# Performance work log

Measured on AMD Instinct MI355X. Metric: run time of the kernel, lower is better.

## Reference

```python
import jax, jax.numpy as jnp
import numpy as np

D, FIN1, CL1_F, CL1_K, CL2_F, CL2_K, FC1_F, FC2_F = 4096, 1, 32, 25, 64, 25, 512, 10
B = 64
NNZ1, NNZ2 = D * 8, (D // 2) * 8
LMAX = 2.0  # lmax_L of a normalized graph Laplacian
FC1FIN = CL2_F * (D // 4)


def setup_inputs() -> dict:
    key = jax.random.key(0)
    ks = jax.random.split(key, 16)
    def lin(kw, fout, fin):
        scale = np.sqrt(2.0 / (fin + fout)).astype(np.float32)
        return jax.random.uniform(kw, (fout, fin), jnp.float32, -scale, scale)
    V2 = D // 2
    return {
        "x": jax.random.normal(ks[0], (B, D, FIN1), jnp.float32),
        "L1_rows": jax.random.randint(ks[1], (NNZ1,), 0, D),
        "L1_cols": jax.random.randint(ks[2], (NNZ1,), 0, D),
        "L1_vals": jax.random.normal(ks[3], (NNZ1,), jnp.float32) * 0.1,
        "L2_rows": jax.random.randint(ks[4], (NNZ2,), 0, V2),
        "L2_cols": jax.random.randint(ks[5], (NNZ2,), 0, V2),
        "L2_vals": jax.random.normal(ks[6], (NNZ2,), jnp.float32) * 0.1,
        "cl1_W": lin(ks[7], CL1_F, CL1_K * FIN1),
        "cl1_b": jnp.zeros((CL1_F,), jnp.float32),
        "cl2_W": lin(ks[8], CL2_F, CL2_K * CL1_F),
        "cl2_b": jnp.zeros((CL2_F,), jnp.float32),
        "fc1_W": lin(ks[9], FC1_F, FC1FIN),
        "fc1_b": jnp.zeros((FC1_F,), jnp.float32),
        "fc2_W": lin(ks[10], FC2_F, FC1_F),
        "fc2_b": jnp.zeros((FC2_F,), jnp.float32),
    }


def _cheby_conv(x, rows, cols, vals, W, b, K):
    # x: [B, V, Fin]; sparse rescaled Laplacian Ls = (2/lmax)*L - I applied as SpMM.
    Bn, V, Fin = x.shape
    x0 = jnp.transpose(x, (1, 2, 0)).reshape(V, Fin * Bn)  # [V, Fin*B]
    coef = jnp.asarray(2.0 / LMAX, x.dtype)

    def Ls(z):  # (2/lmax) * L @ z - z, via segment-sum SpMM
        return coef * jax.ops.segment_sum(vals[:, None] * z[cols], rows, num_segments=V) - z

    xs = [x0]
    if K > 1:
        x1 = Ls(x0)
        xs.append(x1)
    for _ in range(2, K):
        x2 = 2.0 * Ls(x1) - x0
        xs.append(x2)
        x0, x1 = x1, x2
    xk = jnp.stack(xs, 0).reshape(K, V, Fin, Bn)        # [K, V, Fin, B]
    xk = jnp.transpose(xk, (3, 1, 2, 0)).reshape(Bn * V, Fin * K)
    y = xk @ W.T + b
    return y.reshape(Bn, V, -1)


def _max_pool(x, p):
    # max-pool over node dim with stride p (matches MaxPool1d over permuted layout)
    Bn, V, F = x.shape
    return x.reshape(Bn, V // p, p, F).max(axis=2)


def reference(x, L1_rows, L1_cols, L1_vals, L2_rows, L2_cols, L2_vals,
              cl1_W, cl1_b, cl2_W, cl2_b, fc1_W, fc1_b, fc2_W, fc2_b):
    h = _cheby_conv(x, L1_rows, L1_cols, L1_vals, cl1_W, cl1_b, CL1_K)
    h = jax.nn.relu(h)
    h = _max_pool(h, 2)
    h = _cheby_conv(h, L2_rows, L2_cols, L2_vals, cl2_W, cl2_b, CL2_K)
    h = jax.nn.relu(h)
    h = _max_pool(h, 2)
    h = h.reshape(-1, FC1FIN)
    h = jax.nn.relu(h @ fc1_W.T + fc1_b)
    # dropout d=0.0 (eval/deterministic) -> identity
    return h @ fc2_W.T + fc2_b
```

## Files before the change

### kernel.cpp

```cpp
#include <hip/hip_runtime.h>
#include <hip/hip_bf16.h>

#define V1 4096
#define V2 2048
#define NNZ1 32768
#define NNZ2 16384
#define WCAP 48

typedef unsigned short u16;
typedef unsigned int u32;
typedef __attribute__((ext_vector_type(8))) short bf16x8;
typedef __attribute__((ext_vector_type(4))) float f32x4;

static __device__ __forceinline__ float bf2f(u16 u) {
  union { u32 i; float f; } c; c.i = ((u32)u) << 16; return c.f;
}
static __device__ __forceinline__ u16 f2bf(float f) {
  union { u32 i; float f; } c; c.f = f;
  u32 r = c.i + 0x7FFFu + ((c.i >> 16) & 1u);
  return (u16)(r >> 16);
}

__global__ void k_hist(const int* __restrict__ L1r, const int* __restrict__ L2r,
                       const float* __restrict__ W2, u16* __restrict__ Wh,
                       u16* __restrict__ Wl,
                       int* __restrict__ cnt1, int* __restrict__ cnt2) {
  int lt = blockIdx.x, t = threadIdx.x;
  if (lt < 128) {
    atomicAdd(&cnt1[L1r[lt * 256 + t]], 1);
  } else if (lt < 192) {
    atomicAdd(&cnt2[L2r[(lt - 128) * 256 + t]], 1);
  } else {
    int idx = (lt - 192) * 256 + t;
    int f = idx / 800;
    int kap = idx - f * 800;
    int k = kap >> 5, fin = kap & 31;
    float w = W2[f * 800 + fin * 25 + k];
    u16 hi = f2bf(w);
    Wh[idx] = hi;
    Wl[idx] = f2bf(w - bf2f(hi));
  }
}

__global__ void k_scan(int* __restrict__ cnt1, int* __restrict__ rs1,
                       int* __restrict__ cnt2, int* __restrict__ rs2,
                       int* __restrict__ slotOf1, int* __restrict__ rowOf1,
                       int* __restrict__ slotOf2, int* __restrict__ rowOf2) {
  __shared__ int sums[256];
  __shared__ int degS[V1];
  __shared__ int hist[64];
  __shared__ int hb[64];
  int t = threadIdx.x;
  int* cnt; int* rs; int* slotOf; int* rowOf; int V, NT, nnz;
  if (blockIdx.x == 0) { cnt = cnt1; rs = rs1; slotOf = slotOf1; rowOf = rowOf1; V = V1; NT = 1024; nnz = NNZ1; }
  else                 { cnt = cnt2; rs = rs2; slotOf = slotOf2; rowOf = rowOf2; V = V2; NT = 512;  nnz = NNZ2; }
  int chunk = V / 256, base = t * chunk, s = 0;
  for (int i = 0; i < chunk; ++i) { int c = cnt[base + i]; degS[base + i] = c; s += c; }
  sums[t] = s;
  if (t < 64) hist[t] = 0;
  __syncthreads();
  if (t == 0) {
    int run = 0;
    for (int i = 0; i < 256; ++i) { int c = sums[i]; sums[i] = run; run += c; }
  }
  __syncthreads();
  int pfx = sums[t];
  for (int i = 0; i < chunk; ++i) {
    int c = degS[base + i];
    rs[base + i] = pfx;
    cnt[base + i] = pfx;
    pfx += c;
  }
  if (t == 0) rs[V] = nnz;
  for (int i = 0; i < chunk; ++i) {
    int d = degS[base + i]; if (d > 63) d = 63;
    atomicAdd(&hist[d], 1);
  }
  __syncthreads();
  if (t == 0) {
    int run = 0;
    for (int d = 63; d >= 0; --d) { hb[d] = run; run += hist[d]; }
  }
  __syncthreads();
  for (int i = 0; i < chunk; ++i) {
    int v = base + i;
    int d = degS[v]; if (d > 63) d = 63;
    int r = atomicAdd(&hb[d], 1);
    int slot = (r & 3) * NT + (r >> 2);
    slotOf[v] = slot;
    rowOf[slot] = v;
  }
}

__global__ void k_scatter(const int* __restrict__ L1r, const int* __restrict__ L1c,
                          const float* __restrict__ L1v,
                          const int* __restrict__ L2r, const int* __restrict__ L2c,
                          const float* __restrict__ L2v,
                          int* __restrict__ cur1, const int* __restrict__ rs1,
                          const int* __restrict__ slotOf1, float2* __restrict__ ell1,
                          int* __restrict__ cur2, const int* __restrict__ rs2,
                          const int* __restrict__ slotOf2, float2* __restrict__ ell2) {
  int lt = blockIdx.x, t = threadIdx.x;
  if (lt < 128) {
    int e = lt * 256 + t;
    int row = L1r[e];
    int pos = atomicAdd(&cur1[row], 1);
    int w = pos - rs1[row];
    if (w < WCAP)
      ell1[(size_t)w * V1 + slotOf1[row]] = make_float2(L1v[e], __int_as_float(L1c[e] * 4));
  } else {
    int e = (lt - 128) * 256 + t;
    int row = L2r[e];
    int pos = atomicAdd(&cur2[row], 1);
    int w = pos - rs2[row];
    if (w < WCAP)
      ell2[(size_t)w * V2 + slotOf2[row]] = make_float2(L2v[e], __int_as_float(L2c[e] * 16));
  }
}

__global__ void __launch_bounds__(1024) k_l1rec(
    const float* __restrict__ x, const int* __restrict__ rs1,
    const int* __restrict__ rowOf1, const float2* __restrict__ ell1,
    u16* __restrict__ T1) {
  __shared__ float fa[V1];
  const int b = blockIdx.x, t = threadIdx.x;
#pragma unroll
  for (int j = 0; j < 4; ++j) {
    int v = t + j * 1024;
    float xv = x[(size_t)b * V1 + v];
    fa[v] = xv;
    T1[((size_t)b) * V1 + v] = f2bf(xv);
  }
  int vj[4];
#pragma unroll
  for (int j = 0; j < 4; ++j) vj[j] = rowOf1[t + j * 1024];
  int bound = rs1[vj[0] + 1] - rs1[vj[0]];
  if (bound > WCAP) bound = WCAP;
  float t2r[4];
  __syncthreads();
  for (int k = 1; k < 25; ++k) {
    float acc[4] = {0.f, 0.f, 0.f, 0.f};
    for (int w = 0; w < bound; ++w) {
      const float2* ep = ell1 + (size_t)w * V1 + t;
#pragma unroll
      for (int j = 0; j < 4; ++j) {
        float2 ev = ep[j * 1024];
        int ub = __float_as_int(ev.y);
        float av = *(const float*)((const char*)fa + ub);
        acc[j] = fmaf(ev.x, av, acc[j]);
      }
    }
    __syncthreads();
#pragma unroll
    for (int j = 0; j < 4; ++j) {
      float old = fa[vj[j]];
      float z = acc[j] - old;
      if (k > 1) z = 2.f * z - t2r[j];
      t2r[j] = old;
      fa[vj[j]] = z;
    }
    __syncthreads();
#pragma unroll
    for (int j = 0; j < 4; ++j) {
      int v = t + j * 1024;
      T1[((size_t)k * 64 + b) * V1 + v] = f2bf(fa[v]);
    }
  }
}

__global__ void k_conv1(const u16* __restrict__ T1, const float* __restrict__ W1,
                        const float* __restrict__ b1, float* __restrict__ z0) {
  __shared__ float w1s[800];
  __shared__ float b1s[32];
  const int b = blockIdx.x & 63, uc = blockIdx.x >> 6, t = threadIdx.x;
  for (int idx = t; idx < 800; idx += 256) w1s[idx] = W1[idx];
  if (t < 32) b1s[t] = b1[t];
  __syncthreads();
  const int u = uc * 256 + t;
  float a1[25], a2[25];
#pragma unroll
  for (int k = 0; k < 25; ++k) {
    u32 w = *(const u32*)&T1[((size_t)k * 64 + b) * V1 + 2 * u];
    a1[k] = bf2f((u16)w);
    a2[k] = bf2f((u16)(w >> 16));
  }
  float mout[32];
#pragma unroll
  for (int f = 0; f < 32; ++f) {
    float s1 = b1s[f], s2 = b1s[f];
#pragma unroll
    for (int k = 0; k < 25; ++k) {
      float w = w1s[f * 25 + k];
      s1 = fmaf(a1[k], w, s1);
      s2 = fmaf(a2[k], w, s2);
    }
    mout[f] = fmaxf(fmaxf(s1, 0.f), fmaxf(s2, 0.f));
  }
  float4* dst = (float4*)&z0[((size_t)b * V2 + u) * 32];
#pragma unroll
  for (int q = 0; q < 8; ++q)
    dst[q] = make_float4(mout[4 * q], mout[4 * q + 1], mout[4 * q + 2], mout[4 * q + 3]);
}

__global__ void __launch_bounds__(512, 4) k_l2rec(
    const float* __restrict__ z0, const int* __restrict__ rs2,
    const int* __restrict__ rowOf2, const float2* __restrict__ ell2,
    u16* __restrict__ T2, int b0, int bs) {
  __shared__ float TkS[V2 * 4];
  const int bl = blockIdx.x % bs, fg = blockIdx.x / bs;
  const int b = b0 + bl, f0 = fg * 4;
  const int t = threadIdx.x;
  const size_t M = (size_t)bs * V2;
  const size_t mb = (size_t)bl * V2;
#pragma unroll
  for (int j = 0; j < 4; ++j) {
    int v = t + j * 512;
    float4 xv = *(const float4*)&z0[((size_t)b * V2 + v) * 32 + f0];
    *(float4*)&TkS[v * 4] = xv;
    u32 lo = (u32)f2bf(xv.x) | ((u32)f2bf(xv.y) << 16);
    u32 hi = (u32)f2bf(xv.z) | ((u32)f2bf(xv.w) << 16);
    *(uint2*)&T2[((size_t)fg * M + mb + v) * 4] = make_uint2(lo, hi);
  }
  int vj[4];
#pragma unroll
  for (int j = 0; j < 4; ++j) vj[j] = rowOf2[t + j * 512];
  int bound = rs2[vj[0] + 1] - rs2[vj[0]];
  if (bound > WCAP) bound = WCAP;
  float4 t2r[4];
  __syncthreads();
  for (int k = 1; k < 25; ++k) {
    float4 acc[4];
#pragma unroll
    for (int j = 0; j < 4; ++j) acc[j] = make_float4(0.f, 0.f, 0.f, 0.f);
    for (int w = 0; w < bound; ++w) {
      const float2* ep = ell2 + (size_t)w * V2 + t;
#pragma unroll
      for (int j = 0; j < 4; ++j) {
        float2 ev = ep[j * 512];
        int ub = __float_as_int(ev.y);
        float4 tv = *(const float4*)((const char*)TkS + ub);
        acc[j].x = fmaf(ev.x, tv.x, acc[j].x);
        acc[j].y = fmaf(ev.x, tv.y, acc[j].y);
        acc[j].z = fmaf(ev.x, tv.z, acc[j].z);
        acc[j].w = fmaf(ev.x, tv.w, acc[j].w);
      }
    }
    __syncthreads();
#pragma unroll
    for (int j = 0; j < 4; ++j) {
      float4 old = *(const float4*)&TkS[vj[j] * 4];
      float4 z;
      z.x = acc[j].x - old.x; z.y = acc[j].y - old.y;
      z.z = acc[j].z - old.z; z.w = acc[j].w - old.w;
      if (k > 1) {
        z.x = 2.f * z.x - t2r[j].x; z.y = 2.f * z.y - t2r[j].y;
        z.z = 2.f * z.z - t2r[j].z; z.w = 2.f * z.w - t2r[j].w;
      }
      t2r[j] = old;
      *(float4*)&TkS[vj[j] * 4] = z;
    }
    __syncthreads();
#pragma unroll
    for (int j = 0; j < 4; ++j) {
      int v = t + j * 512;
      float4 zz = *(const float4*)&TkS[v * 4];
      u32 lo = (u32)f2bf(zz.x) | ((u32)f2bf(zz.y) << 16);
      u32 hi = (u32)f2bf(zz.z) | ((u32)f2bf(zz.w) << 16);
      *(uint2*)&T2[(((size_t)k * 8 + fg) * M + mb + v) * 4] = make_uint2(lo, hi);
    }
  }
}

__global__ void __launch_bounds__(256) k_conv2mm(
    const u16* __restrict__ T2, const u16* __restrict__ Wh, const u16* __restrict__ Wl,
    const float* __restrict__ b2, float* __restrict__ h2T, int b0, int bs) {
  const int t = threadIdx.x;
  const int wid = t >> 6, lane = t & 63;
  const int ln = lane & 15, kg = lane >> 4;
  const size_t M = (size_t)bs * V2;
  const int mBlk = blockIdx.x * 128;
  const int bl = mBlk >> 11;
  const int v0 = mBlk & (V2 - 1);
  const int m0 = mBlk + wid * 32;
  const int vw = v0 + wid * 32;

  f32x4 acc[2][4];
#pragma unroll
  for (int nt = 0; nt < 4; ++nt) {
    float bv = b2[nt * 16 + ln];
    acc[0][nt] = (f32x4){bv, bv, bv, bv};
    acc[1][nt] = acc[0][nt];
  }

  for (int kc = 0; kc < 25; ++kc) {
    const int coff = kc * 32 + kg * 8;
    bf16x8 bh[4], blo[4];
#pragma unroll
    for (int nt = 0; nt < 4; ++nt) {
      bh[nt]  = *(const bf16x8*)(Wh + (size_t)(nt * 16 + ln) * 800 + coff);
      blo[nt] = *(const bf16x8*)(Wl + (size_t)(nt * 16 + ln) * 800 + coff);
    }
#pragma unroll
    for (int sp = 0; sp < 2; ++sp) {
      const u16* ap = T2 + ((size_t)(kc * 8 + kg * 2) * M + (size_t)(m0 + sp * 16 + ln)) * 4;
      uint2 alo = *(const uint2*)ap;
      uint2 ahi = *(const uint2*)(ap + M * 4);
      union { uint4 u; bf16x8 v; } ac;
      ac.u = make_uint4(alo.x, alo.y, ahi.x, ahi.y);
#pragma unroll
      for (int nt = 0; nt < 4; ++nt) {
        acc[sp][nt] = __builtin_amdgcn_mfma_f32_16x16x32_bf16(ac.v, bh[nt], acc[sp][nt], 0, 0, 0);
        acc[sp][nt] = __builtin_amdgcn_mfma_f32_16x16x32_bf16(ac.v, blo[nt], acc[sp][nt], 0, 0, 0);
      }
    }
  }
  const int b = b0 + bl;
#pragma unroll
  for (int sp = 0; sp < 2; ++sp) {
    int u = ((vw + sp * 16) >> 1) + kg * 2;
#pragma unroll
    for (int nt = 0; nt < 4; ++nt) {
      int f = nt * 16 + ln;
      float p0 = fmaxf(fmaxf(acc[sp][nt].x, acc[sp][nt].y), 0.f);
      float p1 = fmaxf(fmaxf(acc[sp][nt].z, acc[sp][nt].w), 0.f);
      h2T[((size_t)u * 64 + f) * 64 + b] = p0;
      h2T[((size_t)(u + 1) * 64 + f) * 64 + b] = p1;
    }
  }
}

__global__ void k_fc1(const float* __restrict__ h2T, const float* __restrict__ fW1,
                      float* __restrict__ fc1o) {
  __shared__ float wS[16 * 256];
  const int jt = blockIdx.x & 31, ks = blockIdx.x >> 5;
  const int j0 = jt * 16, k0 = ks * 2048;
  const int t = threadIdx.x;
  const int b = t & 63, jl = t >> 6;
  float acc[4] = {0.f, 0.f, 0.f, 0.f};
  for (int kc = 0; kc < 8; ++kc) {
    int kbase = k0 + kc * 256;
    __syncthreads();
    for (int fi = t; fi < 1024; fi += 256) {
      int rowj = fi >> 6, colq = fi & 63;
      *(float4*)&wS[rowj * 256 + colq * 4] =
          *(const float4*)&fW1[(size_t)(j0 + rowj) * 65536 + kbase + colq * 4];
    }
    __syncthreads();
    for (int kl = 0; kl < 256; ++kl) {
      float hv = h2T[(size_t)(kbase + kl) * 64 + b];
#pragma unroll
      for (int q = 0; q < 4; ++q) acc[q] = fmaf(hv, wS[(jl * 4 + q) * 256 + kl], acc[q]);
    }
  }
#pragma unroll
  for (int q = 0; q < 4; ++q) atomicAdd(&fc1o[(j0 + jl * 4 + q) * 64 + b], acc[q]);
}

__global__ void k_fc2(const float* __restrict__ fc1o, const float* __restrict__ fb1,
                      const float* __restrict__ fW2, const float* __restrict__ fb2,
                      float* __restrict__ out) {
  const int c = blockIdx.x, b = threadIdx.x;
  float s = fb2[c];
  for (int j = 0; j < 512; ++j) {
    float a = fmaxf(fc1o[j * 64 + b] + fb1[j], 0.f);
    s = fmaf(a, fW2[c * 512 + j], s);
  }
  out[b * 10 + c] = s;
}

extern "C" void kernel_launch(void* const* d_in, const int* in_sizes, int n_in,
                              void* d_out, int out_size, void* d_ws, size_t ws_size,
                              hipStream_t stream) {
  const float* x    = (const float*)d_in[0];
  const int* L1r    = (const int*)d_in[1];
  const int* L1c    = (const int*)d_in[2];
  const float* L1v  = (const float*)d_in[3];
  const int* L2r    = (const int*)d_in[4];
  const int* L2c    = (const int*)d_in[5];
  const float* L2v  = (const float*)d_in[6];
  const float* W1   = (const float*)d_in[7];
  const float* b1   = (const float*)d_in[8];
  const float* W2   = (const float*)d_in[9];
  const float* b2   = (const float*)d_in[10];
  const float* fW1  = (const float*)d_in[11];
  const float* fb1  = (const float*)d_in[12];
  const float* fW2  = (const float*)d_in[13];
  const float* fb2  = (const float*)d_in[14];
  float* out = (float*)d_out;

  float* Wf = (float*)d_ws;
  size_t off = 0;
  auto alloc = [&](size_t n) { float* q = Wf + off; off += n; return q; };
  int* cnt1    = (int*)alloc(4096);
  int* rs1     = (int*)alloc(4104);
  int* cnt2    = (int*)alloc(2048);
  int* rs2     = (int*)alloc(2056);
  int* slotOf1 = (int*)alloc(4096);
  int* rowOf1  = (int*)alloc(4096);
  int* slotOf2 = (int*)alloc(2048);
  int* rowOf2  = (int*)alloc(2048);
  u16* Wh      = (u16*)alloc(25600);
  u16* Wl      = (u16*)alloc(25600);
  float* fc1o  = alloc(32768);
  float2* ell1 = (float2*)alloc((size_t)WCAP * V1 * 2);
  float2* ell2 = (float2*)alloc((size_t)WCAP * V2 * 2);
  float* z0    = alloc(4194304);
  float* h2T   = alloc(4194304);
  size_t fixedB = off * 4;

  int ns = 8;
  for (int c = 1; c <= 8; c <<= 1) {
    size_t t2b = (size_t)V2 * (64 / c) * 800 * 2;
    size_t big = t2b > 16777216ull ? t2b : 16777216ull;
    if (fixedB + big + 65536 <= ws_size) { ns = c; break; }
  }
  const int bs = 64 / ns;
  u16* T1 = (u16*)(Wf + off);
  u16* T2 = (u16*)(Wf + off);

  hipMemsetAsync(cnt1, 0, 4096 * sizeof(int), stream);
  hipMemsetAsync(cnt2, 0, 2048 * sizeof(int), stream);
  hipMemsetAsync(fc1o, 0, 32768 * sizeof(float), stream);
  hipMemsetAsync(ell1, 0, (size_t)WCAP * V1 * 8, stream);
  hipMemsetAsync(ell2, 0, (size_t)WCAP * V2 * 8, stream);

  k_hist<<<392, 256, 0, stream>>>(L1r, L2r, W2, Wh, Wl, cnt1, cnt2);
  k_scan<<<2, 256, 0, stream>>>(cnt1, rs1, cnt2, rs2, slotOf1, rowOf1, slotOf2, rowOf2);
  k_scatter<<<192, 256, 0, stream>>>(L1r, L1c, L1v, L2r, L2c, L2v,
                                     cnt1, rs1, slotOf1, ell1,
                                     cnt2, rs2, slotOf2, ell2);

  k_l1rec<<<64, 1024, 0, stream>>>(x, rs1, rowOf1, ell1, T1);
  k_conv1<<<512, 256, 0, stream>>>(T1, W1, b1, z0);

  for (int s = 0; s < ns; ++s) {
    int b0 = s * bs;
    k_l2rec<<<bs * 8, 512, 0, stream>>>(z0, rs2, rowOf2, ell2, T2, b0, bs);
    k_conv2mm<<<bs * 16, 256, 0, stream>>>(T2, Wh, Wl, b2, h2T, b0, bs);
  }

  k_fc1<<<1024, 256, 0, stream>>>(h2T, fW1, fc1o);
  k_fc2<<<10, 64, 0, stream>>>(fc1o, fb1, fW2, fb2, out);
}
```

Before: 792.9 us.

## Store pooled conv2 output batch-major and stage fc1 activations in shared memory

Result: slower. 846.9 us (+6.8%).

```diff
diff --git a/kernel.cpp b/kernel.cpp
--- a/kernel.cpp
+++ b/kernel.cpp
@@ -273,7 +273,7 @@
 
 __global__ void __launch_bounds__(256) k_conv2mm(
     const u16* __restrict__ T2, const u16* __restrict__ Wh, const u16* __restrict__ Wl,
-    const float* __restrict__ b2, float* __restrict__ h2T, int b0, int bs) {
+    const float* __restrict__ b2, float* __restrict__ h2, int b0, int bs) {
   const int t = threadIdx.x;
   const int wid = t >> 6, lane = t & 63;
   const int ln = lane & 15, kg = lane >> 4;
@@ -315,6 +315,7 @@
     }
   }
   const int b = b0 + bl;
+  float* hrow = h2 + (size_t)b * 65536;
 #pragma unroll
   for (int sp = 0; sp < 2; ++sp) {
     int u = ((vw + sp * 16) >> 1) + kg * 2;
@@ -323,49 +324,61 @@
       int f = nt * 16 + ln;
       float p0 = fmaxf(fmaxf(acc[sp][nt].x, acc[sp][nt].y), 0.f);
       float p1 = fmaxf(fmaxf(acc[sp][nt].z, acc[sp][nt].w), 0.f);
-      h2T[((size_t)u * 64 + f) * 64 + b] = p0;
-      h2T[((size_t)(u + 1) * 64 + f) * 64 + b] = p1;
-    }
-  }
-}
-
-__global__ void k_fc1(const float* __restrict__ h2T, const float* __restrict__ fW1,
-                      float* __restrict__ fc1o) {
-  __shared__ float wS[16 * 256];
+      hrow[(size_t)u * 64 + f] = p0;
+      hrow[(size_t)(u + 1) * 64 + f] = p1;
+    }
+  }
+}
+
+__global__ void __launch_bounds__(256) k_fc1(
+    const float* __restrict__ h2, const float* __restrict__ fW1,
+    float* __restrict__ fc1o) {
+  __shared__ float wS[16 * 128];
+  __shared__ float hS[64 * 129];
   const int jt = blockIdx.x & 31, ks = blockIdx.x >> 5;
   const int j0 = jt * 16, k0 = ks * 2048;
   const int t = threadIdx.x;
   const int b = t & 63, jl = t >> 6;
   float acc[4] = {0.f, 0.f, 0.f, 0.f};
-  for (int kc = 0; kc < 8; ++kc) {
-    int kbase = k0 + kc * 256;
-    __syncthreads();
-    for (int fi = t; fi < 1024; fi += 256) {
-      int rowj = fi >> 6, colq = fi & 63;
-      *(float4*)&wS[rowj * 256 + colq * 4] =
-          *(const float4*)&fW1[(size_t)(j0 + rowj) * 65536 + kbase + colq * 4];
-    }
-    __syncthreads();
-    for (int kl = 0; kl < 256; ++kl) {
-      float hv = h2T[(size_t)(kbase + kl) * 64 + b];
-#pragma unroll
-      for (int q = 0; q < 4; ++q) acc[q] = fmaf(hv, wS[(jl * 4 + q) * 256 + kl], acc[q]);
+  for (int kc = 0; kc < 16; ++kc) {
+    int kbase = k0 + kc * 128;
+    __syncthreads();
+    for (int fi = t; fi < 2048; fi += 256) {
+      int rowj = fi >> 7, col = fi & 127;
+      wS[rowj * 128 + col] = fW1[(size_t)(j0 + rowj) * 65536 + kbase + col];
+    }
+    for (int fi = t; fi < 8192; fi += 256) {
+      int bb = fi >> 7, kl = fi & 127;
+      hS[bb * 129 + kl] = h2[(size_t)bb * 65536 + kbase + kl];
+    }
+    __syncthreads();
+    for (int kl = 0; kl < 128; ++kl) {
+      float hv = hS[b * 129 + kl];
+#pragma unroll
+      for (int q = 0; q < 4; ++q) acc[q] = fmaf(hv, wS[(jl * 4 + q) * 128 + kl], acc[q]);
     }
   }
 #pragma unroll
   for (int q = 0; q < 4; ++q) atomicAdd(&fc1o[(j0 + jl * 4 + q) * 64 + b], acc[q]);
 }
 
-__global__ void k_fc2(const float* __restrict__ fc1o, const float* __restrict__ fb1,
-                      const float* __restrict__ fW2, const float* __restrict__ fb2,
-                      float* __restrict__ out) {
-  const int c = blockIdx.x, b = threadIdx.x;
-  float s = fb2[c];
-  for (int j = 0; j < 512; ++j) {
+__global__ void __launch_bounds__(256) k_fc2(
+    const float* __restrict__ fc1o, const float* __restrict__ fb1,
+    const float* __restrict__ fW2, const float* __restrict__ fb2,
+    float* __restrict__ out) {
+  __shared__ float red[256];
+  const int c = blockIdx.x, t = threadIdx.x;
+  const int b = t & 63, g = t >> 6;
+  float s = 0.f;
+  for (int j = g * 128; j < g * 128 + 128; ++j) {
     float a = fmaxf(fc1o[j * 64 + b] + fb1[j], 0.f);
     s = fmaf(a, fW2[c * 512 + j], s);
   }
-  out[b * 10 + c] = s;
+  red[t] = s;
+  __syncthreads();
+  if (t < 64) {
+    out[b * 10 + c] = red[t] + red[t + 64] + red[t + 128] + red[t + 192] + fb2[c];
+  }
 }
 
 extern "C" void kernel_launch(void* const* d_in, const int* in_sizes, int n_in,
@@ -405,7 +418,7 @@
   float2* ell1 = (float2*)alloc((size_t)WCAP * V1 * 2);
   float2* ell2 = (float2*)alloc((size_t)WCAP * V2 * 2);
   float* z0    = alloc(4194304);
-  float* h2T   = alloc(4194304);
+  float* h2    = alloc(4194304);
   size_t fixedB = off * 4;
 
   int ns = 8;
@@ -436,9 +449,9 @@
   for (int s = 0; s < ns; ++s) {
     int b0 = s * bs;
     k_l2rec<<<bs * 8, 512, 0, stream>>>(z0, rs2, rowOf2, ell2, T2, b0, bs);
-    k_conv2mm<<<bs * 16, 256, 0, stream>>>(T2, Wh, Wl, b2, h2T, b0, bs);
-  }
-
-  k_fc1<<<1024, 256, 0, stream>>>(h2T, fW1, fc1o);
-  k_fc2<<<10, 64, 0, stream>>>(fc1o, fb1, fW2, fb2, out);
-}
+    k_conv2mm<<<bs * 16, 256, 0, stream>>>(T2, Wh, Wl, b2, h2, b0, bs);
+  }
+
+  k_fc1<<<1024, 256, 0, stream>>>(h2, fW1, fc1o);
+  k_fc2<<<10, 256, 0, stream>>>(fc1o, fb1, fW2, fb2, out);
+}
```
